# Kernel optimization log

Measured on AMD Instinct MI355X. Metric: run time of the kernel, lower is better.

Reference implementation:

```python
import jax, jax.numpy as jnp
import numpy as np

B, S, D, H = 4, 2048, 1024, 16
HD = D // H


def setup_inputs() -> dict:
    key = jax.random.key(0)
    ks = jax.random.split(key, 5)
    scale = 0.02
    return {
        "x": jax.random.normal(ks[0], (B, S, D), dtype=jnp.float32),
        "Wq": jax.random.normal(ks[1], (D, D), dtype=jnp.float32) * scale,
        "Wk": jax.random.normal(ks[2], (D, D), dtype=jnp.float32) * scale,
        "Wv": jax.random.normal(ks[3], (D, D), dtype=jnp.float32) * scale,
        "Wo": jax.random.normal(ks[4], (D, D), dtype=jnp.float32) * scale,
    }


def reference(x, Wq, Wk, Wv, Wo):
    b, s, d = x.shape
    # Linear layers (torch Linear: y = x @ W.T), no bias
    q = jnp.einsum('bsd,ed->bse', x, Wq).reshape(b, s, H, HD).transpose(0, 2, 1, 3)
    k = jnp.einsum('bsd,ed->bse', x, Wk).reshape(b, s, H, HD).transpose(0, 2, 1, 3)
    v = jnp.einsum('bsd,ed->bse', x, Wv).reshape(b, s, H, HD).transpose(0, 2, 1, 3)
    # [B,H,S,S] attention scores
    scores = jnp.einsum('bhqd,bhkd->bhqk', q, k)
    causal = jnp.tril(jnp.ones((s, s), dtype=bool))
    scores = jnp.where(causal, scores, -jnp.inf)
    # faithful to source: mask first, then scale, then softmax
    weights = jax.nn.softmax(scores / jnp.sqrt(jnp.float32(HD)), axis=-1)
    # dropout p=0.0 (eval): identity
    ctx = jnp.einsum('bhqk,bhkd->bhqd', weights, v)
    ctx = ctx.transpose(0, 2, 1, 3).reshape(b, s, d)
    return jnp.einsum('bsd,ed->bse', ctx, Wo)
```

## Files before the change

kernel.cpp:

```cpp
#include <hip/hip_runtime.h>
#include <math.h>

typedef unsigned short u16;
typedef __attribute__((ext_vector_type(8))) short short8;
typedef __attribute__((ext_vector_type(4))) float f32x4;
typedef __attribute__((ext_vector_type(16))) float f32x16;
typedef __attribute__((ext_vector_type(4))) unsigned int u32x4;

constexpr int Bb = 4, S_LEN = 2048, DMODEL = 1024, NH = 16;
constexpr int MTOT = Bb * S_LEN;

#define QSCALE 0.18033688011112042f

__device__ __forceinline__ u16 f2bf(float f) {
    union { float f; unsigned u; } v; v.f = f;
    unsigned r = v.u + 0x7FFFu + ((v.u >> 16) & 1u);
    return (u16)(r >> 16);
}

__device__ __forceinline__ float exp2_fast(float x) {
#if __has_builtin(__builtin_amdgcn_exp2f)
    return __builtin_amdgcn_exp2f(x);
#else
    float r; asm("v_exp_f32 %0, %1" : "=v"(r) : "v"(x)); return r;
#endif
}

__device__ __forceinline__ unsigned pk_bf16(float s0, float s1) {
    unsigned pk;
    asm("v_cvt_pk_bf16_f32 %0, %1, %2" : "=v"(pk) : "v"(s0), "v"(s1));
    return pk;
}

__device__ __forceinline__ void load_lds16(const void* g, void* l) {
    __builtin_amdgcn_global_load_lds(
        (const __attribute__((address_space(1))) unsigned int*)g,
        (__attribute__((address_space(3))) unsigned int*)l, 16, 0, 0);
}

__global__ __launch_bounds__(256)
void cvt_all(const float* __restrict__ x,
             const float* __restrict__ w0, const float* __restrict__ w1,
             const float* __restrict__ w2, const float* __restrict__ w3,
             u16* __restrict__ xb, u16* __restrict__ b0, u16* __restrict__ b1,
             u16* __restrict__ b2, u16* __restrict__ b3)
{
    int gid = blockIdx.x * 256 + threadIdx.x;
    constexpr int NXo = (MTOT * DMODEL) / 8;
    constexpr int NWo = (DMODEL * DMODEL) / 8;
    const float* s; u16* d; int o;
    float sc = 1.0f;
    if (gid < NXo) { s = x; d = xb; o = gid; }
    else {
        int t = gid - NXo;
        int w = t >> 17;
        o = t & (NWo - 1);
        s = (w == 0) ? w0 : (w == 1) ? w1 : (w == 2) ? w2 : w3;
        d = (w == 0) ? b0 : (w == 1) ? b1 : (w == 2) ? b2 : b3;
        if (w == 0) sc = QSCALE;
    }
    const float4* sp = (const float4*)(s + (size_t)o * 8);
    float4 a = sp[0], bq = sp[1];
    short8 ov;
    ov[0] = (short)f2bf(a.x * sc);  ov[1] = (short)f2bf(a.y * sc);
    ov[2] = (short)f2bf(a.z * sc);  ov[3] = (short)f2bf(a.w * sc);
    ov[4] = (short)f2bf(bq.x * sc); ov[5] = (short)f2bf(bq.y * sc);
    ov[6] = (short)f2bf(bq.z * sc); ov[7] = (short)f2bf(bq.w * sc);
    *(short8*)(d + (size_t)o * 8) = ov;
}

__global__ __launch_bounds__(256, 2)
void gemm_bt(const u16* __restrict__ X,
             const u16* __restrict__ W0, const u16* __restrict__ W1, const u16* __restrict__ W2,
             u16* __restrict__ Y0, u16* __restrict__ Y1,
             u16* __restrict__ VT,
             int M, int N, int K)
{
    const u16* W = (blockIdx.z == 0) ? W0 : (blockIdx.z == 1) ? W1 : W2;

    __shared__ __align__(16) u16 lds[2 * 128 * 64];
    u16* lA = lds;
    u16* lB = lds + 128 * 64;

    const int tid  = threadIdx.x;
    const int wave = tid >> 6;
    const int lane = tid & 63;
    const int qd   = lane >> 4;
    const int c    = lane & 15;
    const int tm   = blockIdx.x * 128;
    const int tn   = blockIdx.y * 128;
    const int wm   = (wave >> 1) * 64;
    const int wn   = (wave & 1) * 64;

    f32x4 acc[4][4] = {};

    for (int k0 = 0; k0 < K; k0 += 64) {
        if (k0) __syncthreads();
#pragma unroll
        for (int it = 0; it < 4; ++it) {
            int chunk = it * 256 + tid;
            int row = chunk >> 3, hc = chunk & 7;
            load_lds16(X + (size_t)(tm + row) * K + k0 + hc * 8,
                       (char*)lA + (it * 256 + wave * 64) * 16);
            load_lds16(W + (size_t)(tn + row) * K + k0 + hc * 8,
                       (char*)lB + (it * 256 + wave * 64) * 16);
        }
        __syncthreads();

#pragma unroll
        for (int kk = 0; kk < 64; kk += 32) {
            short8 a[4], b[4];
#pragma unroll
            for (int i = 0; i < 4; ++i) {
                a[i] = *(const short8*)&lA[(wm + i * 16 + c) * 64 + kk + qd * 8];
                b[i] = *(const short8*)&lB[(wn + i * 16 + c) * 64 + kk + qd * 8];
            }
#pragma unroll
            for (int mi = 0; mi < 4; ++mi)
#pragma unroll
                for (int ni = 0; ni < 4; ++ni)
                    acc[mi][ni] = __builtin_amdgcn_mfma_f32_16x16x32_bf16(
                        a[mi], b[ni], acc[mi][ni], 0, 0, 0);
        }
    }

    if (blockIdx.z != 2) {
        u16* Y = (blockIdx.z == 0) ? Y0 : Y1;
#pragma unroll
        for (int mi = 0; mi < 4; ++mi)
#pragma unroll
            for (int ni = 0; ni < 4; ++ni)
#pragma unroll
                for (int r = 0; r < 4; r += 2) {
                    unsigned pk = pk_bf16(acc[mi][ni][r], acc[mi][ni][r + 1]);
                    int row = tm + wm + mi * 16 + qd * 4 + r;
                    int col = tn + wn + ni * 16 + c;
                    Y[(size_t)row * N + col]       = (u16)(pk & 0xffffu);
                    Y[(size_t)(row + 1) * N + col] = (u16)(pk >> 16);
                }
    } else {
        __syncthreads();
        u16* Tw = lds + wave * 4096;
#pragma unroll
        for (int mi = 0; mi < 4; ++mi)
#pragma unroll
            for (int ni = 0; ni < 4; ++ni)
#pragma unroll
                for (int r = 0; r < 4; r += 2) {
                    unsigned pk = pk_bf16(acc[mi][ni][r], acc[mi][ni][r + 1]);
                    int r0 = mi * 16 + qd * 4 + r;
                    int cl = ni * 16 + c;
                    Tw[r0 * 64       + (cl ^ ((r0 << 1) & 0x38))]        = (u16)(pk & 0xffffu);
                    Tw[(r0 + 1) * 64 + (cl ^ (((r0 + 1) << 1) & 0x38))]  = (u16)(pk >> 16);
                }
        asm volatile("s_waitcnt lgkmcnt(0)" ::: "memory");

        const int b2   = tm >> 11;
        const int smb  = (tm & 2047) + wm;
        const int hgl  = (tn + wn) >> 6;
        const int sc8  = lane & 7;
#pragma unroll
        for (int it = 0; it < 8; ++it) {
            int hd = it * 8 + (lane >> 3);
            short8 o;
#pragma unroll
            for (int jj = 0; jj < 8; ++jj) {
                int rr = sc8 * 8 + jj;
                o[jj] = (short)Tw[rr * 64 + (hd ^ ((rr << 1) & 0x38))];
            }
            *(short8*)&VT[(size_t)((b2 * 16 + hgl) * 64 + hd) * S_LEN + smb + sc8 * 8] = o;
        }
    }
}

__global__ __launch_bounds__(256, 2)
void gemm_bt_f32(const u16* __restrict__ X, const u16* __restrict__ W,
                 float* __restrict__ Y, int M, int N, int K)
{
    __shared__ __align__(16) u16 lA[128 * 64];
    __shared__ __align__(16) u16 lB[128 * 64];

    const int tid  = threadIdx.x;
    const int wave = tid >> 6;
    const int lane = tid & 63;
    const int qd   = lane >> 4;
    const int c    = lane & 15;
    const int tm   = blockIdx.x * 128;
    const int tn   = blockIdx.y * 128;
    const int wm   = (wave >> 1) * 64;
    const int wn   = (wave & 1) * 64;

    f32x4 acc[4][4] = {};

    for (int k0 = 0; k0 < K; k0 += 64) {
        if (k0) __syncthreads();
#pragma unroll
        for (int it = 0; it < 4; ++it) {
            int chunk = it * 256 + tid;
            int row = chunk >> 3, hc = chunk & 7;
            load_lds16(X + (size_t)(tm + row) * K + k0 + hc * 8,
                       (char*)lA + (it * 256 + wave * 64) * 16);
            load_lds16(W + (size_t)(tn + row) * K + k0 + hc * 8,
                       (char*)lB + (it * 256 + wave * 64) * 16);
        }
        __syncthreads();

#pragma unroll
        for (int kk = 0; kk < 64; kk += 32) {
            short8 a[4], b[4];
#pragma unroll
            for (int i = 0; i < 4; ++i) {
                a[i] = *(const short8*)&lA[(wm + i * 16 + c) * 64 + kk + qd * 8];
                b[i] = *(const short8*)&lB[(wn + i * 16 + c) * 64 + kk + qd * 8];
            }
#pragma unroll
            for (int mi = 0; mi < 4; ++mi)
#pragma unroll
                for (int ni = 0; ni < 4; ++ni)
                    acc[mi][ni] = __builtin_amdgcn_mfma_f32_16x16x32_bf16(
                        a[mi], b[ni], acc[mi][ni], 0, 0, 0);
        }
    }

#pragma unroll
    for (int mi = 0; mi < 4; ++mi)
#pragma unroll
        for (int ni = 0; ni < 4; ++ni)
#pragma unroll
            for (int r = 0; r < 4; ++r) {
                int row = tm + wm + mi * 16 + qd * 4 + r;
                int col = tn + wn + ni * 16 + c;
                Y[(size_t)row * N + col] = acc[mi][ni][r];
            }
}

__global__ __launch_bounds__(512, 2)
void attention(const u16* __restrict__ Q, const u16* __restrict__ K,
               const u16* __restrict__ VT, u16* __restrict__ CTX)
{
    const int i  = blockIdx.x;
    const int j  = i & 255;
    const int bh = j >> 2;
    const int t  = j & 3;
    const int qt = (i >> 8) ? t : (7 - t);
    const int b = bh >> 4, h = bh & 15;

    __shared__ __align__(16) u16 lK[2][64 * 64];
    __shared__ __align__(16) u16 lV[2][64 * 64];

    const int tid = threadIdx.x, wave = tid >> 6, lane = tid & 63;
    const int l31 = lane & 31, hi = lane >> 5;
    const int wrow = wave * 32;
    const int srow = tid >> 3, shc = tid & 7;
    const int shcs = shc ^ (srow & 7);
    const int rxk  = l31 & 7;
    const size_t kbase = (size_t)(b * S_LEN) * DMODEL + h * 64;
    const size_t vbase = (size_t)(bh * 64) * S_LEN;

    const int q0 = qt * 256;
    const int nkv = 4 * qt + 4;
    const int qrg = q0 + wrow + l31;

    short8 qf[4];
#pragma unroll
    for (int ks = 0; ks < 4; ++ks)
        qf[ks] = *(const short8*)&Q[(size_t)(b * S_LEN + qrg) * DMODEL
                                    + h * 64 + ks * 16 + hi * 8];

    f32x16 oacc0 = {}, oacc1 = {};
    float psum = 0.f;

    load_lds16(K + kbase + (size_t)srow * DMODEL + shcs * 8,
               (char*)lK[0] + wave * 1024);
    load_lds16(VT + vbase + (size_t)srow * S_LEN + shcs * 8,
               (char*)lV[0] + wave * 1024);

    for (int kt = 0; kt < nkv; ++kt) {
        const int cur = kt & 1;
        const int k0 = kt * 64;

        __builtin_amdgcn_s_barrier();
        if (kt + 1 < nkv) {
            const int kn = (kt + 1) * 64;
            load_lds16(K + kbase + (size_t)(kn + srow) * DMODEL + shcs * 8,
                       (char*)lK[cur ^ 1] + wave * 1024);
            load_lds16(VT + vbase + (size_t)srow * S_LEN + kn + shcs * 8,
                       (char*)lV[cur ^ 1] + wave * 1024);
            asm volatile("s_waitcnt vmcnt(2)" ::: "memory");
        } else {
            asm volatile("s_waitcnt vmcnt(0)" ::: "memory");
        }
        __builtin_amdgcn_sched_barrier(0);
        __builtin_amdgcn_s_barrier();
        __builtin_amdgcn_sched_barrier(0);

        if (k0 <= q0 + wrow + 31) {
            f32x16 s0 = {}, s1 = {};
            __builtin_amdgcn_s_setprio(1);
#pragma unroll
            for (int hs = 0; hs < 4; ++hs) {
                const int sl = ((hs * 2 + hi) ^ rxk) << 3;
                short8 kf0 = *(const short8*)&lK[cur][l31 * 64 + sl];
                short8 kf1 = *(const short8*)&lK[cur][(32 + l31) * 64 + sl];
                s0 = __builtin_amdgcn_mfma_f32_32x32x16_bf16(kf0, qf[hs], s0, 0, 0, 0);
                s1 = __builtin_amdgcn_mfma_f32_32x32x16_bf16(kf1, qf[hs], s1, 0, 0, 0);
            }
            __builtin_amdgcn_s_setprio(0);

            float pva[16], pvb[16];
            if (k0 + 63 > q0 + wrow) {
                const int lim = qrg - k0 - 4 * hi;
#pragma unroll
                for (int r = 0; r < 16; ++r) {
                    const int ka = (r & 3) + 8 * (r >> 2);
                    pva[r] = (ka > lim)      ? -1.0e38f : s0[r];
                    pvb[r] = (ka + 32 > lim) ? -1.0e38f : s1[r];
                }
            } else {
#pragma unroll
                for (int r = 0; r < 16; ++r) { pva[r] = s0[r]; pvb[r] = s1[r]; }
            }
#pragma unroll
            for (int r = 0; r < 16; ++r) {
                pva[r] = exp2_fast(fminf(pva[r], 86.0f));
                pvb[r] = exp2_fast(fminf(pvb[r], 86.0f));
                psum += pva[r] + pvb[r];
            }
            unsigned own0[8], own1[8];
#pragma unroll
            for (int q = 0; q < 8; ++q) {
                own0[q] = pk_bf16(pva[2 * q], pva[2 * q + 1]);
                own1[q] = pk_bf16(pvb[2 * q], pvb[2 * q + 1]);
            }

            short8 paf[4];
#pragma unroll
            for (int f = 0; f < 4; ++f) {
                const unsigned* own = (f < 2) ? own0 : own1;
                const int base = (f & 1) * 4;
                unsigned a0 = own[base + 0], b0 = own[base + 2];
                unsigned a1 = own[base + 1], b1 = own[base + 3];
                asm("v_permlane32_swap_b32 %0, %1" : "+v"(a0), "+v"(b0));
                asm("v_permlane32_swap_b32 %0, %1" : "+v"(a1), "+v"(b1));
                u32x4 w; w[0] = a0; w[1] = a1; w[2] = b0; w[3] = b1;
                paf[f] = __builtin_bit_cast(short8, w);
            }

            __builtin_amdgcn_s_setprio(1);
#pragma unroll
            for (int ks = 0; ks < 4; ++ks) {
                const int vsl = ((ks * 2 + hi) ^ rxk) << 3;
                short8 vf0 = *(const short8*)&lV[cur][l31 * 64 + vsl];
                short8 vf1 = *(const short8*)&lV[cur][(32 + l31) * 64 + vsl];
                oacc0 = __builtin_amdgcn_mfma_f32_32x32x16_bf16(paf[ks], vf0, oacc0, 0, 0, 0);
                oacc1 = __builtin_amdgcn_mfma_f32_32x32x16_bf16(paf[ks], vf1, oacc1, 0, 0, 0);
            }
            __builtin_amdgcn_s_setprio(0);
        }
    }

    float pt = psum + __shfl_xor(psum, 32);
#pragma unroll
    for (int r = 0; r < 16; ++r) {
        const int orow = (r & 3) + 8 * (r >> 2) + 4 * hi;
        float inv = 1.0f / __shfl(pt, orow);
        const int rowg = q0 + wrow + orow;
        size_t base = (size_t)(b * S_LEN + rowg) * DMODEL + h * 64;
        unsigned pk = pk_bf16(oacc0[r] * inv, oacc1[r] * inv);
        CTX[base + l31]      = (u16)(pk & 0xffffu);
        CTX[base + 32 + l31] = (u16)(pk >> 16);
    }
}

extern "C" void kernel_launch(void* const* d_in, const int* in_sizes, int n_in,
                              void* d_out, int out_size, void* d_ws, size_t ws_size,
                              hipStream_t stream)
{
    const size_t MB = 1024 * 1024;
    char* ws = (char*)d_ws;
    if (ws_size < 72 * MB + 64) return;

    u16* xb  = (u16*)ws;
    u16* wb0 = (u16*)(ws + 16 * MB);
    u16* wb1 = (u16*)(ws + 18 * MB);
    u16* wb2 = (u16*)(ws + 20 * MB);
    u16* wb3 = (u16*)(ws + 22 * MB);
    u16* q   = (u16*)(ws + 24 * MB);
    u16* k   = (u16*)(ws + 40 * MB);
    u16* vt  = (u16*)(ws + 56 * MB);
    u16* ctx = xb;
    float* out = (float*)d_out;

    constexpr int NCVT = (MTOT * DMODEL + 4 * DMODEL * DMODEL) / 8 / 256;

    cvt_all<<<NCVT, 256, 0, stream>>>(
        (const float*)d_in[0], (const float*)d_in[1], (const float*)d_in[2],
        (const float*)d_in[3], (const float*)d_in[4], xb, wb0, wb1, wb2, wb3);

    gemm_bt<<<dim3(MTOT / 128, DMODEL / 128, 3), 256, 0, stream>>>(
        xb, wb0, wb1, wb2, q, k, vt, MTOT, DMODEL, DMODEL);
    attention<<<512, 512, 0, stream>>>(q, k, vt, ctx);
    gemm_bt_f32<<<dim3(MTOT / 128, DMODEL / 128, 1), 256, 0, stream>>>(
        ctx, wb3, out, MTOT, DMODEL, DMODEL);
}
```

Baseline: 245.2 us.

## Fuse Q, K, V projection GEMMs into one kernel sharing the X tile

Merges the three z-indexed projection launches into a single kernel where each block loads the X tile once and multiplies it against the Wq, Wk and Wv tiles, keeping three accumulator sets. This removes redundant global and LDS loads of X and shrinks the grid. In exchange, register pressure triples for the accumulators, LDS per block grows to 64KB, and the grid has a third as many blocks, which may hurt occupancy or cause spills.

```diff
diff --git a/kernel.cpp b/kernel.cpp
--- a/kernel.cpp
+++ b/kernel.cpp
@@ -70,17 +70,16 @@
 }
 
 __global__ __launch_bounds__(256, 2)
-void gemm_bt(const u16* __restrict__ X,
-             const u16* __restrict__ W0, const u16* __restrict__ W1, const u16* __restrict__ W2,
-             u16* __restrict__ Y0, u16* __restrict__ Y1,
-             u16* __restrict__ VT,
-             int M, int N, int K)
+void gemm_qkv(const u16* __restrict__ X,
+              const u16* __restrict__ W0, const u16* __restrict__ W1, const u16* __restrict__ W2,
+              u16* __restrict__ Qo, u16* __restrict__ Ko, u16* __restrict__ VT,
+              int M, int N, int K)
 {
-    const u16* W = (blockIdx.z == 0) ? W0 : (blockIdx.z == 1) ? W1 : W2;
-
-    __shared__ __align__(16) u16 lds[2 * 128 * 64];
-    u16* lA = lds;
-    u16* lB = lds + 128 * 64;
+    __shared__ __align__(16) u16 lds[4 * 128 * 64];
+    u16* lA  = lds;
+    u16* lB0 = lds + 128 * 64;
+    u16* lB1 = lds + 2 * 128 * 64;
+    u16* lB2 = lds + 3 * 128 * 64;
 
     const int tid  = threadIdx.x;
     const int wave = tid >> 6;
@@ -92,7 +91,7 @@
     const int wm   = (wave >> 1) * 64;
     const int wn   = (wave & 1) * 64;
 
-    f32x4 acc[4][4] = {};
+    f32x4 acc0[4][4] = {}, acc1[4][4] = {}, acc2[4][4] = {};
 
     for (int k0 = 0; k0 < K; k0 += 64) {
         if (k0) __syncthreads();
@@ -100,10 +99,13 @@
         for (int it = 0; it < 4; ++it) {
             int chunk = it * 256 + tid;
             int row = chunk >> 3, hc = chunk & 7;
-            load_lds16(X + (size_t)(tm + row) * K + k0 + hc * 8,
-                       (char*)lA + (it * 256 + wave * 64) * 16);
-            load_lds16(W + (size_t)(tn + row) * K + k0 + hc * 8,
-                       (char*)lB + (it * 256 + wave * 64) * 16);
+            size_t ga = (size_t)(tm + row) * K + k0 + hc * 8;
+            size_t gb = (size_t)(tn + row) * K + k0 + hc * 8;
+            int ldo = (it * 256 + wave * 64) * 16;
+            load_lds16(X  + ga, (char*)lA  + ldo);
+            load_lds16(W0 + gb, (char*)lB0 + ldo);
+            load_lds16(W1 + gb, (char*)lB1 + ldo);
+            load_lds16(W2 + gb, (char*)lB2 + ldo);
         }
         __syncthreads();
 
@@ -111,65 +113,93 @@
         for (int kk = 0; kk < 64; kk += 32) {
             short8 a[4], b[4];
 #pragma unroll
-            for (int i = 0; i < 4; ++i) {
+            for (int i = 0; i < 4; ++i)
                 a[i] = *(const short8*)&lA[(wm + i * 16 + c) * 64 + kk + qd * 8];
-                b[i] = *(const short8*)&lB[(wn + i * 16 + c) * 64 + kk + qd * 8];
-            }
+#pragma unroll
+            for (int i = 0; i < 4; ++i)
+                b[i] = *(const short8*)&lB0[(wn + i * 16 + c) * 64 + kk + qd * 8];
 #pragma unroll
             for (int mi = 0; mi < 4; ++mi)
 #pragma unroll
                 for (int ni = 0; ni < 4; ++ni)
-                    acc[mi][ni] = __builtin_amdgcn_mfma_f32_16x16x32_bf16(
-                        a[mi], b[ni], acc[mi][ni], 0, 0, 0);
-        }
-    }
-
-    if (blockIdx.z != 2) {
-        u16* Y = (blockIdx.z == 0) ? Y0 : Y1;
-#pragma unroll
-        for (int mi = 0; mi < 4; ++mi)
-#pragma unroll
-            for (int ni = 0; ni < 4; ++ni)
-#pragma unroll
-                for (int r = 0; r < 4; r += 2) {
-                    unsigned pk = pk_bf16(acc[mi][ni][r], acc[mi][ni][r + 1]);
-                    int row = tm + wm + mi * 16 + qd * 4 + r;
-                    int col = tn + wn + ni * 16 + c;
-                    Y[(size_t)row * N + col]       = (u16)(pk & 0xffffu);
-                    Y[(size_t)(row + 1) * N + col] = (u16)(pk >> 16);
-                }
-    } else {
-        __syncthreads();
-        u16* Tw = lds + wave * 4096;
-#pragma unroll
-        for (int mi = 0; mi < 4; ++mi)
-#pragma unroll
-            for (int ni = 0; ni < 4; ++ni)
-#pragma unroll
-                for (int r = 0; r < 4; r += 2) {
-                    unsigned pk = pk_bf16(acc[mi][ni][r], acc[mi][ni][r + 1]);
-                    int r0 = mi * 16 + qd * 4 + r;
-                    int cl = ni * 16 + c;
-                    Tw[r0 * 64       + (cl ^ ((r0 << 1) & 0x38))]        = (u16)(pk & 0xffffu);
-                    Tw[(r0 + 1) * 64 + (cl ^ (((r0 + 1) << 1) & 0x38))]  = (u16)(pk >> 16);
-                }
-        asm volatile("s_waitcnt lgkmcnt(0)" ::: "memory");
-
-        const int b2   = tm >> 11;
-        const int smb  = (tm & 2047) + wm;
-        const int hgl  = (tn + wn) >> 6;
-        const int sc8  = lane & 7;
-#pragma unroll
-        for (int it = 0; it < 8; ++it) {
-            int hd = it * 8 + (lane >> 3);
-            short8 o;
-#pragma unroll
-            for (int jj = 0; jj < 8; ++jj) {
-                int rr = sc8 * 8 + jj;
-                o[jj] = (short)Tw[rr * 64 + (hd ^ ((rr << 1) & 0x38))];
-            }
-            *(short8*)&VT[(size_t)((b2 * 16 + hgl) * 64 + hd) * S_LEN + smb + sc8 * 8] = o;
-        }
+                    acc0[mi][ni] = __builtin_amdgcn_mfma_f32_16x16x32_bf16(
+                        a[mi], b[ni], acc0[mi][ni], 0, 0, 0);
+#pragma unroll
+            for (int i = 0; i < 4; ++i)
+                b[i] = *(const short8*)&lB1[(wn + i * 16 + c) * 64 + kk + qd * 8];
+#pragma unroll
+            for (int mi = 0; mi < 4; ++mi)
+#pragma unroll
+                for (int ni = 0; ni < 4; ++ni)
+                    acc1[mi][ni] = __builtin_amdgcn_mfma_f32_16x16x32_bf16(
+                        a[mi], b[ni], acc1[mi][ni], 0, 0, 0);
+#pragma unroll
+            for (int i = 0; i < 4; ++i)
+                b[i] = *(const short8*)&lB2[(wn + i * 16 + c) * 64 + kk + qd * 8];
+#pragma unroll
+            for (int mi = 0; mi < 4; ++mi)
+#pragma unroll
+                for (int ni = 0; ni < 4; ++ni)
+                    acc2[mi][ni] = __builtin_amdgcn_mfma_f32_16x16x32_bf16(
+                        a[mi], b[ni], acc2[mi][ni], 0, 0, 0);
+        }
+    }
+
+#pragma unroll
+    for (int mi = 0; mi < 4; ++mi)
+#pragma unroll
+        for (int ni = 0; ni < 4; ++ni)
+#pragma unroll
+            for (int r = 0; r < 4; r += 2) {
+                unsigned pk = pk_bf16(acc0[mi][ni][r], acc0[mi][ni][r + 1]);
+                int row = tm + wm + mi * 16 + qd * 4 + r;
+                int col = tn + wn + ni * 16 + c;
+                Qo[(size_t)row * N + col]       = (u16)(pk & 0xffffu);
+                Qo[(size_t)(row + 1) * N + col] = (u16)(pk >> 16);
+            }
+#pragma unroll
+    for (int mi = 0; mi < 4; ++mi)
+#pragma unroll
+        for (int ni = 0; ni < 4; ++ni)
+#pragma unroll
+            for (int r = 0; r < 4; r += 2) {
+                unsigned pk = pk_bf16(acc1[mi][ni][r], acc1[mi][ni][r + 1]);
+                int row = tm + wm + mi * 16 + qd * 4 + r;
+                int col = tn + wn + ni * 16 + c;
+                Ko[(size_t)row * N + col]       = (u16)(pk & 0xffffu);
+                Ko[(size_t)(row + 1) * N + col] = (u16)(pk >> 16);
+            }
+
+    __syncthreads();
+    u16* Tw = lds + wave * 4096;
+#pragma unroll
+    for (int mi = 0; mi < 4; ++mi)
+#pragma unroll
+        for (int ni = 0; ni < 4; ++ni)
+#pragma unroll
+            for (int r = 0; r < 4; r += 2) {
+                unsigned pk = pk_bf16(acc2[mi][ni][r], acc2[mi][ni][r + 1]);
+                int r0 = mi * 16 + qd * 4 + r;
+                int cl = ni * 16 + c;
+                Tw[r0 * 64       + (cl ^ ((r0 << 1) & 0x38))]        = (u16)(pk & 0xffffu);
+                Tw[(r0 + 1) * 64 + (cl ^ (((r0 + 1) << 1) & 0x38))]  = (u16)(pk >> 16);
+            }
+    asm volatile("s_waitcnt lgkmcnt(0)" ::: "memory");
+
+    const int b2   = tm >> 11;
+    const int smb  = (tm & 2047) + wm;
+    const int hgl  = (tn + wn) >> 6;
+    const int sc8  = lane & 7;
+#pragma unroll
+    for (int it = 0; it < 8; ++it) {
+        int hd = it * 8 + (lane >> 3);
+        short8 o;
+#pragma unroll
+        for (int jj = 0; jj < 8; ++jj) {
+            int rr = sc8 * 8 + jj;
+            o[jj] = (short)Tw[rr * 64 + (hd ^ ((rr << 1) & 0x38))];
+        }
+        *(short8*)&VT[(size_t)((b2 * 16 + hgl) * 64 + hd) * S_LEN + smb + sc8 * 8] = o;
     }
 }
 
@@ -397,7 +427,7 @@
         (const float*)d_in[0], (const float*)d_in[1], (const float*)d_in[2],
         (const float*)d_in[3], (const float*)d_in[4], xb, wb0, wb1, wb2, wb3);
 
-    gemm_bt<<<dim3(MTOT / 128, DMODEL / 128, 3), 256, 0, stream>>>(
+    gemm_qkv<<<dim3(MTOT / 128, DMODEL / 128), 256, 0, stream>>>(
         xb, wb0, wb1, wb2, q, k, vt, MTOT, DMODEL, DMODEL);
     attention<<<512, 512, 0, stream>>>(q, k, vt, ctx);
     gemm_bt_f32<<<dim3(MTOT / 128, DMODEL / 128, 1), 256, 0, stream>>>(
```

Measured after the change: 318.8 us. +30.0%, slower.
